# Optimization experiments

Measured on AMD Instinct MI355X. Metric: run time of the kernel, lower is better.

Reference implementation:

```python
import jax, jax.numpy as jnp
import numpy as np

BS, D, L, H = 8, 256, 1024, 8
DK = D // H
EPS = 1e-8


def setup_inputs() -> dict:
    key = jax.random.key(0)
    ks = jax.random.split(key, 9)
    queries = jax.random.normal(ks[0], (BS, D, L), jnp.float32)
    keys = jax.random.normal(ks[1], (BS, D, L), jnp.float32)
    values = jax.random.normal(ks[2], (BS, D, L), jnp.float32)
    # binary float mask over positions, (bs, L, 1) as the module expects
    mask = (jax.random.uniform(ks[3], (BS, L, 1)) > 0.1).astype(jnp.float32)
    # grouped 1x1 conv weights: one (dk, dk) block per head (xavier-ish scale)
    wscale = np.sqrt(2.0 / (DK + DK)).astype(np.float32)
    Wq = jax.random.normal(ks[4], (H, DK, DK), jnp.float32) * wscale
    Wk = jax.random.normal(ks[5], (H, DK, DK), jnp.float32) * wscale
    Wv = jax.random.normal(ks[6], (H, DK, DK), jnp.float32) * wscale
    # full 1x1 conv projection
    Wp = jax.random.normal(ks[7], (D, D), jnp.float32) * np.sqrt(1.0 / D).astype(np.float32)
    bp = jnp.zeros((D,), jnp.float32)
    return {"queries": queries, "keys": keys, "values": values, "mask": mask,
            "Wq": Wq, "Wk": Wk, "Wv": Wv, "Wp": Wp, "bp": bp}


def _grouped_conv1x1(x, W):
    # x: (bs, D, L) viewed as (bs, H, dk, L); W: (H, dk_out, dk_in)
    bs, _, l = x.shape
    xh = x.reshape(bs, H, DK, l)
    return jnp.einsum('hij,bhjl->bhil', W, xh)  # (bs, H, dk, L)


def _masked_softmax(logits, mask4):
    # logits: (bs, H, L, L); mask4: (bs, 1, 1, L) -- faithful to module's custom softmax
    max_value = jax.lax.stop_gradient(jnp.max(logits * mask4, axis=-1, keepdims=True))
    z = (logits - max_value) * mask4
    m = jnp.exp(z) * mask4
    n = jnp.sum(m, axis=-1, keepdims=True)
    p_mask = mask4 * jnp.swapaxes(mask4, 2, 3)  # (bs, 1, L, L)
    return p_mask * (m / (n + EPS))


def reference(queries, keys, values, mask, Wq, Wk, Wv, Wp, bp):
    bs, c, l = queries.shape
    m = jnp.swapaxes(mask, 1, 2)          # (bs, 1, L)
    m4 = m[:, :, None, :]                  # (bs, 1, 1, L)
    q = _grouped_conv1x1(queries, Wq) * m4  # (bs, H, dk, L)
    k = _grouped_conv1x1(keys, Wk) * m4
    v = _grouped_conv1x1(values, Wv)
    # attn[b,h,d,e] = sum_c q[b,h,c,d] k[b,h,c,e]  (no 1/sqrt(dk) scaling, as in source)
    attn = jnp.einsum('bhcd,bhce->bhde', q, k)
    atn = _masked_softmax(attn, m4)
    # value[b,h,c,k] = sum_d atn[b,h,k,d] * (v*mask)[b,h,c,d]
    val = jnp.einsum('bhkd,bhcd->bhck', atn, v * m4)
    val = val.reshape(bs, c, l)
    out = jnp.einsum('ij,bjl->bil', Wp, val) + bp[None, :, None]
    return jnp.swapaxes(out * m, 1, 2)      # (bs, L, D)
```

## Files before the change

kernel.cpp:

```cpp
#include <hip/hip_runtime.h>
#include <math.h>


constexpr int cD  = 256;
constexpr int cL  = 1024;
constexpr int cH  = 8;
constexpr int cDK = 32;

typedef __attribute__((ext_vector_type(8))) short s8v;
typedef __attribute__((ext_vector_type(4))) float f4v;
typedef unsigned int u32;
typedef unsigned short u16;

static __device__ __forceinline__ u32 rne_hi(float x) {
    u32 u = __float_as_uint(x);
    return u + 0x7fffu + ((u >> 16) & 1u);
}
static __device__ __forceinline__ u32 pack_bf2(float a, float b) {
    return __builtin_amdgcn_perm(rne_hi(b), rne_hi(a), 0x07060302u);
}
static __device__ __forceinline__ u16 f2bf(float x) { return (u16)(rne_hi(x) >> 16); }
static __device__ __forceinline__ float bf2f(u16 h) { return __uint_as_float(((u32)h) << 16); }

__global__ __launch_bounds__(256, 4) void proj_kv_kernel(
    const float* __restrict__ keys, const float* __restrict__ values,
    const float* __restrict__ mask, const float* __restrict__ Wk,
    const float* __restrict__ Wv, u16* __restrict__ kp_hi,
    u16* __restrict__ kp_lo, u16* __restrict__ vp_bf)
{
    __shared__ __align__(16) float xs[32][68];
    __shared__ __align__(16) float wT[32][36];
    __shared__ float msl[64];

    const int t   = threadIdx.x;
    const int bid = blockIdx.x;
    const int lt  = bid & 15;
    const int h   = (bid >> 4) & 7;
    const int b   = bid >> 7;
    const int l0  = lt * 64;

    if (t < 64) msl[t] = mask[b * cL + l0 + t];

    for (int idx = t; idx < 512; idx += 256) {
        int j = idx >> 4, l4 = (idx & 15) * 4;
        *reinterpret_cast<float4*>(&xs[j][l4]) =
            *reinterpret_cast<const float4*>(&keys[(b * cD + h * cDK + j) * cL + l0 + l4]);
    }
    for (int idx = t; idx < 1024; idx += 256) {
        int c = idx >> 5, j = idx & 31;
        wT[j][c] = Wk[(h * cDK + c) * cDK + j];
    }
    __syncthreads();
    {
        const int l = t & 63, ig = t >> 6;
        float acc[8] = {0, 0, 0, 0, 0, 0, 0, 0};
        #pragma unroll
        for (int j = 0; j < 32; ++j) {
            float xv = xs[j][l];
            float4 w0 = *reinterpret_cast<const float4*>(&wT[j][ig * 8]);
            float4 w1 = *reinterpret_cast<const float4*>(&wT[j][ig * 8 + 4]);
            acc[0] += w0.x * xv; acc[1] += w0.y * xv;
            acc[2] += w0.z * xv; acc[3] += w0.w * xv;
            acc[4] += w1.x * xv; acc[5] += w1.y * xv;
            acc[6] += w1.z * xv; acc[7] += w1.w * xv;
        }
        float mk = msl[l];
        s8v hv, lv;
        #pragma unroll
        for (int i = 0; i < 8; ++i) {
            float kv = acc[i] * mk;
            u16 hh = f2bf(kv);
            hv[i] = (short)hh;
            lv[i] = (short)f2bf(kv - bf2f(hh));
        }
        size_t off = (((size_t)(b * cH + h)) * cL + l0 + l) * cDK + ig * 8;
        *reinterpret_cast<s8v*>(&kp_hi[off]) = hv;
        *reinterpret_cast<s8v*>(&kp_lo[off]) = lv;
    }
    __syncthreads();

    for (int idx = t; idx < 512; idx += 256) {
        int j = idx >> 4, l4 = (idx & 15) * 4;
        *reinterpret_cast<float4*>(&xs[j][l4]) =
            *reinterpret_cast<const float4*>(&values[(b * cD + h * cDK + j) * cL + l0 + l4]);
    }
    for (int idx = t; idx < 1024; idx += 256) {
        int c = idx >> 5, j = idx & 31;
        wT[j][c] = Wv[(h * cDK + c) * cDK + j];
    }
    __syncthreads();
    {
        const int l4 = (t & 15) * 4;
        const int c0 = (t >> 4) * 2;
        float a0[4] = {0, 0, 0, 0}, a1[4] = {0, 0, 0, 0};
        #pragma unroll
        for (int j = 0; j < 32; ++j) {
            float4 xv = *reinterpret_cast<const float4*>(&xs[j][l4]);
            float w0 = wT[j][c0], w1 = wT[j][c0 + 1];
            a0[0] += w0 * xv.x; a0[1] += w0 * xv.y; a0[2] += w0 * xv.z; a0[3] += w0 * xv.w;
            a1[0] += w1 * xv.x; a1[1] += w1 * xv.y; a1[2] += w1 * xv.z; a1[3] += w1 * xv.w;
        }
        size_t base = ((size_t)(b * cH + h)) * cDK;
        uint2 v0 = make_uint2(pack_bf2(a0[0], a0[1]), pack_bf2(a0[2], a0[3]));
        uint2 v1 = make_uint2(pack_bf2(a1[0], a1[1]), pack_bf2(a1[2], a1[3]));
        *reinterpret_cast<uint2*>(&vp_bf[(base + c0) * cL + l0 + l4])     = v0;
        *reinterpret_cast<uint2*>(&vp_bf[(base + c0 + 1) * cL + l0 + l4]) = v1;
    }
}

__global__ __launch_bounds__(256, 3) void attn_kernel(
    const float* __restrict__ queries, const float* __restrict__ mask,
    const float* __restrict__ Wq, const u16* __restrict__ kp_hi,
    const u16* __restrict__ kp_lo, const u16* __restrict__ vp_bf,
    u16* __restrict__ val_bf)
{
    __shared__ __align__(16) u16 ksbuf[2][2][2048];
    __shared__ __align__(16) u16 qsb[2][2048];
    __shared__ __align__(16) u16 vsbuf[2][2304];
    __shared__ __align__(16) u32 pb32[2304];
    __shared__ __align__(16) float msbuf[2][64];

    const int t     = threadIdx.x;
    const int bid   = blockIdx.x;
    const int strip = bid & 15;
    const int h     = (bid >> 4) & 7;
    const int b     = bid >> 7;
    const int r0    = strip * 64;
    const int lane  = t & 63;
    const int w     = t >> 6;
    const int ln15  = lane & 15;
    const int lq    = lane >> 4;

    float* qtmp = reinterpret_cast<float*>(&ksbuf[0][0][0]);
    float* wqt  = reinterpret_cast<float*>((char*)&ksbuf[0][0][0] + 8704);
    {
        int j = t >> 3, f8 = (t & 7) * 8;
        const float* src = &queries[(b * cD + h * cDK + j) * cL + r0 + f8];
        float4 v0 = *reinterpret_cast<const float4*>(src);
        float4 v1 = *reinterpret_cast<const float4*>(src + 4);
        *reinterpret_cast<float4*>(&qtmp[j * 68 + f8])     = v0;
        *reinterpret_cast<float4*>(&qtmp[j * 68 + f8 + 4]) = v1;
    }
    {
        int c = t >> 3, j4 = (t & 7) * 4;
        float4 wv = *reinterpret_cast<const float4*>(&Wq[(h * cDK + c) * cDK + j4]);
        wqt[(j4 + 0) * 32 + c] = wv.x; wqt[(j4 + 1) * 32 + c] = wv.y;
        wqt[(j4 + 2) * 32 + c] = wv.z; wqt[(j4 + 3) * 32 + c] = wv.w;
    }
    __syncthreads();

    {
        float acc[8] = {0, 0, 0, 0, 0, 0, 0, 0};
        #pragma unroll
        for (int j = 0; j < 32; ++j) {
            float xv = qtmp[j * 68 + lane];
            float4 w0 = *reinterpret_cast<const float4*>(&wqt[j * 32 + w * 8]);
            float4 w1 = *reinterpret_cast<const float4*>(&wqt[j * 32 + w * 8 + 4]);
            acc[0] += w0.x * xv; acc[1] += w0.y * xv;
            acc[2] += w0.z * xv; acc[3] += w0.w * xv;
            acc[4] += w1.x * xv; acc[5] += w1.y * xv;
            acc[6] += w1.z * xv; acc[7] += w1.w * xv;
        }
        s8v hv, lv;
        #pragma unroll
        for (int i = 0; i < 8; ++i) {
            u16 hh = f2bf(acc[i]);
            hv[i] = (short)hh;
            lv[i] = (short)f2bf(acc[i] - bf2f(hh));
        }
        *reinterpret_cast<s8v*>(&qsb[0][lane * 32 + w * 8]) = hv;
        *reinterpret_cast<s8v*>(&qsb[1][lane * 32 + w * 8]) = lv;
    }
    __syncthreads();

    const size_t kvbase = ((size_t)(b * cH + h)) * 32768;
    const int se = t >> 2, sc = (t & 3) * 8;
    const int vc = t >> 3, ve = (t & 7) * 8;

    {
        s8v kh = *reinterpret_cast<const s8v*>(&kp_hi[kvbase + se * 32 + sc]);
        s8v kl = *reinterpret_cast<const s8v*>(&kp_lo[kvbase + se * 32 + sc]);
        *reinterpret_cast<s8v*>(&ksbuf[0][0][se * 32 + sc]) = kh;
        *reinterpret_cast<s8v*>(&ksbuf[0][1][se * 32 + sc]) = kl;
        s8v vv = *reinterpret_cast<const s8v*>(&vp_bf[kvbase + vc * 1024 + ve]);
        *reinterpret_cast<s8v*>(&vsbuf[0][vc * 72 + ve]) = vv;
        if (t < 64) msbuf[0][t] = mask[b * cL + t];
    }

    const s8v qh = *reinterpret_cast<const s8v*>(&qsb[0][(w * 16 + ln15) * 32 + lq * 8]);
    const s8v ql = *reinterpret_cast<const s8v*>(&qsb[1][(w * 16 + ln15) * 32 + lq * 8]);

    f4v o0 = {0.f, 0.f, 0.f, 0.f}, o1 = {0.f, 0.f, 0.f, 0.f};
    float mo = -INFINITY, lr = 0.f;
    const int pbrow = (w * 16 + ln15) * 36;
    const int ksoff = ln15 * 32 + lq * 8;
    const int vsoff = ln15 * 72 + lq * 8;

    for (int et = 0; et < 16; ++et) {
        __syncthreads();
        const int pp = et & 1;
        const bool pre = (et < 15);
        s8v khp, klp, vvp; float msp = 0.f;
        if (pre) {
            const int e0n = (et + 1) * 64;
            khp = *reinterpret_cast<const s8v*>(&kp_hi[kvbase + (e0n + se) * 32 + sc]);
            klp = *reinterpret_cast<const s8v*>(&kp_lo[kvbase + (e0n + se) * 32 + sc]);
            vvp = *reinterpret_cast<const s8v*>(&vp_bf[kvbase + vc * 1024 + e0n + ve]);
            if (t < 64) msp = mask[b * cL + e0n + t];
        }

        f4v sA[4];
        #pragma unroll
        for (int es = 0; es < 4; ++es) {
            const s8v kh = *reinterpret_cast<const s8v*>(&ksbuf[pp][0][es * 512 + ksoff]);
            const s8v kl = *reinterpret_cast<const s8v*>(&ksbuf[pp][1][es * 512 + ksoff]);
            f4v a = {0.f, 0.f, 0.f, 0.f};
            a = __builtin_amdgcn_mfma_f32_16x16x32_bf16(kh, qh, a, 0, 0, 0);
            a = __builtin_amdgcn_mfma_f32_16x16x32_bf16(kl, qh, a, 0, 0, 0);
            a = __builtin_amdgcn_mfma_f32_16x16x32_bf16(kh, ql, a, 0, 0, 0);
            sA[es] = a;
        }

        float tm = fmaxf(fmaxf(fmaxf(sA[0][0], sA[0][1]), fmaxf(sA[0][2], sA[0][3])),
                   fmaxf(fmaxf(fmaxf(sA[1][0], sA[1][1]), fmaxf(sA[1][2], sA[1][3])),
                   fmaxf(fmaxf(fmaxf(sA[2][0], sA[2][1]), fmaxf(sA[2][2], sA[2][3])),
                         fmaxf(fmaxf(sA[3][0], sA[3][1]), fmaxf(sA[3][2], sA[3][3])))));
        tm = fmaxf(tm, __shfl_xor(tm, 16));
        tm = fmaxf(tm, __shfl_xor(tm, 32));
        const float mn = fmaxf(mo, tm);
        const float al = __expf(mo - mn);
        mo = mn;
        o0[0] *= al; o0[1] *= al; o0[2] *= al; o0[3] *= al;
        o1[0] *= al; o1[1] *= al; o1[2] *= al; o1[3] *= al;

        float ps = 0.f;
        #pragma unroll
        for (int es = 0; es < 4; ++es) {
            float4 mk4 = *reinterpret_cast<const float4*>(&msbuf[pp][es * 16 + lq * 4]);
            float p0 = __expf((sA[es][0] - mn) * mk4.x) * mk4.x;
            float p1 = __expf((sA[es][1] - mn) * mk4.y) * mk4.y;
            float p2 = __expf((sA[es][2] - mn) * mk4.z) * mk4.z;
            float p3 = __expf((sA[es][3] - mn) * mk4.w) * mk4.w;
            ps += (p0 + p1) + (p2 + p3);
            uint2 pk = make_uint2(pack_bf2(p0, p1), pack_bf2(p2, p3));
            *reinterpret_cast<uint2*>(&pb32[pbrow + es * 8 + lq * 2]) = pk;
        }
        ps += __shfl_xor(ps, 16);
        ps += __shfl_xor(ps, 32);
        lr = lr * al + ps;

        #pragma unroll
        for (int ch = 0; ch < 2; ++ch) {
            s8v pB  = *reinterpret_cast<const s8v*>(
                          reinterpret_cast<const u16*>(&pb32[pbrow + ch * 16 + lq * 4]));
            s8v vA0 = *reinterpret_cast<const s8v*>(&vsbuf[pp][vsoff + ch * 32]);
            s8v vA1 = *reinterpret_cast<const s8v*>(&vsbuf[pp][vsoff + ch * 32 + 1152]);
            o0 = __builtin_amdgcn_mfma_f32_16x16x32_bf16(vA0, pB, o0, 0, 0, 0);
            o1 = __builtin_amdgcn_mfma_f32_16x16x32_bf16(vA1, pB, o1, 0, 0, 0);
        }

        if (pre) {
            const int bn = pp ^ 1;
            *reinterpret_cast<s8v*>(&ksbuf[bn][0][se * 32 + sc]) = khp;
            *reinterpret_cast<s8v*>(&ksbuf[bn][1][se * 32 + sc]) = klp;
            *reinterpret_cast<s8v*>(&vsbuf[bn][vc * 72 + ve]) = vvp;
            if (t < 64) msbuf[bn][t] = msp;
        }
    }

    {
        const float linv = 1.0f / (lr + 1e-8f);
        const size_t obase = ((size_t)(b * cL + r0 + w * 16 + ln15)) * cD + h * cDK;
        uint2 q0 = make_uint2(pack_bf2(o0[0] * linv, o0[1] * linv),
                              pack_bf2(o0[2] * linv, o0[3] * linv));
        uint2 q1 = make_uint2(pack_bf2(o1[0] * linv, o1[1] * linv),
                              pack_bf2(o1[2] * linv, o1[3] * linv));
        *reinterpret_cast<uint2*>(&val_bf[obase + lq * 4])      = q0;
        *reinterpret_cast<uint2*>(&val_bf[obase + 16 + lq * 4]) = q1;
    }
}

__global__ __launch_bounds__(256, 2) void outproj_kernel(
    const u16* __restrict__ val_bf, const float* __restrict__ Wp,
    const float* __restrict__ bp, const float* __restrict__ mask,
    float* __restrict__ out)
{
    __shared__ __align__(16) u16 vt[64 * 264];
    __shared__ __align__(16) u16 wpb[64 * 264];
    __shared__ float mrow[64];

    const int t    = threadIdx.x;
    const int bid  = blockIdx.x;
    const int it   = bid & 3;
    const int lt   = (bid >> 2) & 15;
    const int b    = bid >> 6;
    const int l0   = lt * 64, i0 = it * 64;
    const int lane = t & 63, w = t >> 6, ln15 = lane & 15, lq = lane >> 4;

    {
        int row = t >> 2, seg = (t & 3) * 64;
        const u16* src = &val_bf[((size_t)(b * cL + l0 + row)) * cD + seg];
        #pragma unroll
        for (int k = 0; k < 4; ++k) {
            s8v a0 = *reinterpret_cast<const s8v*>(src + k * 16);
            s8v a1 = *reinterpret_cast<const s8v*>(src + k * 16 + 8);
            *reinterpret_cast<s8v*>(&vt[row * 264 + seg + k * 16])     = a0;
            *reinterpret_cast<s8v*>(&vt[row * 264 + seg + k * 16 + 8]) = a1;
        }
    }
    {
        int row = t >> 2, seg = (t & 3) * 64;
        const float* src = &Wp[((size_t)(i0 + row)) * cD + seg];
        #pragma unroll
        for (int k = 0; k < 8; ++k) {
            float4 f0 = *reinterpret_cast<const float4*>(src + k * 8);
            float4 f1 = *reinterpret_cast<const float4*>(src + k * 8 + 4);
            uint4 pk = make_uint4(pack_bf2(f0.x, f0.y), pack_bf2(f0.z, f0.w),
                                  pack_bf2(f1.x, f1.y), pack_bf2(f1.z, f1.w));
            *reinterpret_cast<uint4*>(&wpb[row * 264 + seg + k * 8]) = pk;
        }
    }
    if (t < 64) mrow[t] = mask[b * cL + l0 + t];
    __syncthreads();

    f4v acc[4] = {{0.f, 0.f, 0.f, 0.f}, {0.f, 0.f, 0.f, 0.f},
                  {0.f, 0.f, 0.f, 0.f}, {0.f, 0.f, 0.f, 0.f}};
    #pragma unroll
    for (int kc = 0; kc < 8; ++kc) {
        s8v aA = *reinterpret_cast<const s8v*>(&vt[(w * 16 + ln15) * 264 + kc * 32 + lq * 8]);
        #pragma unroll
        for (int ti = 0; ti < 4; ++ti) {
            s8v bB = *reinterpret_cast<const s8v*>(&wpb[(ti * 16 + ln15) * 264 + kc * 32 + lq * 8]);
            acc[ti] = __builtin_amdgcn_mfma_f32_16x16x32_bf16(aA, bB, acc[ti], 0, 0, 0);
        }
    }

    float mk[4];
    #pragma unroll
    for (int rg = 0; rg < 4; ++rg) mk[rg] = mrow[w * 16 + lq * 4 + rg];
    #pragma unroll
    for (int ti = 0; ti < 4; ++ti) {
        float bpv = bp[i0 + ti * 16 + ln15];
        #pragma unroll
        for (int rg = 0; rg < 4; ++rg) {
            int l = l0 + w * 16 + lq * 4 + rg;
            out[((size_t)(b * cL + l)) * cD + i0 + ti * 16 + ln15] =
                (acc[ti][rg] + bpv) * mk[rg];
        }
    }
}

extern "C" void kernel_launch(void* const* d_in, const int* in_sizes, int n_in,
                              void* d_out, int out_size, void* d_ws, size_t ws_size,
                              hipStream_t stream) {
    const float* queries = (const float*)d_in[0];
    const float* keys    = (const float*)d_in[1];
    const float* values  = (const float*)d_in[2];
    const float* mask    = (const float*)d_in[3];
    const float* Wq      = (const float*)d_in[4];
    const float* Wk      = (const float*)d_in[5];
    const float* Wv      = (const float*)d_in[6];
    const float* Wp      = (const float*)d_in[7];
    const float* bp      = (const float*)d_in[8];
    float* out = (float*)d_out;

    char* wsb = (char*)d_ws;
    u16* kp_hi  = (u16*)(wsb);
    u16* kp_lo  = (u16*)(wsb + (4u << 20));
    u16* vp_bf  = (u16*)(wsb + (8u << 20));
    u16* val_bf = (u16*)(wsb + (12u << 20));

    proj_kv_kernel<<<dim3(1024), dim3(256), 0, stream>>>(keys, values, mask, Wk, Wv,
                                                         kp_hi, kp_lo, vp_bf);
    attn_kernel<<<dim3(1024), dim3(256), 0, stream>>>(queries, mask, Wq,
                                                      kp_hi, kp_lo, vp_bf, val_bf);
    outproj_kernel<<<dim3(512), dim3(256), 0, stream>>>(val_bf, Wp, bp, mask, out);
}
```

Baseline: 145.0 us.

## Switch attention pipeline from split bf16 hi/lo to single fp16 MFMA

Replaces the bf16 hi+lo split representation of Q and K (three MFMAs per score tile) with a single fp16 representation and one f16 MFMA per tile. This drops the kp_lo buffer and its loads and stores, and converts V, P, val and Wp to fp16. It also restructures the shared-memory layout into one padded arena, preloads the full mask row once, and raises the attention kernel's occupancy hint from 3 to 4. fp16 has less exponent range than bf16, and the unscaled logits now carry less precision than the compensated split did, so accuracy may degrade.

```diff
diff --git a/kernel.cpp b/kernel.cpp
--- a/kernel.cpp
+++ b/kernel.cpp
@@ -7,26 +7,16 @@
 constexpr int cH  = 8;
 constexpr int cDK = 32;
 
-typedef __attribute__((ext_vector_type(8))) short s8v;
+typedef _Float16 f16;
+typedef __attribute__((ext_vector_type(8))) _Float16 h8;
+typedef __attribute__((ext_vector_type(4))) _Float16 h4;
 typedef __attribute__((ext_vector_type(4))) float f4v;
-typedef unsigned int u32;
-typedef unsigned short u16;
-
-static __device__ __forceinline__ u32 rne_hi(float x) {
-    u32 u = __float_as_uint(x);
-    return u + 0x7fffu + ((u >> 16) & 1u);
-}
-static __device__ __forceinline__ u32 pack_bf2(float a, float b) {
-    return __builtin_amdgcn_perm(rne_hi(b), rne_hi(a), 0x07060302u);
-}
-static __device__ __forceinline__ u16 f2bf(float x) { return (u16)(rne_hi(x) >> 16); }
-static __device__ __forceinline__ float bf2f(u16 h) { return __uint_as_float(((u32)h) << 16); }
 
 __global__ __launch_bounds__(256, 4) void proj_kv_kernel(
     const float* __restrict__ keys, const float* __restrict__ values,
     const float* __restrict__ mask, const float* __restrict__ Wk,
-    const float* __restrict__ Wv, u16* __restrict__ kp_hi,
-    u16* __restrict__ kp_lo, u16* __restrict__ vp_bf)
+    const float* __restrict__ Wv, f16* __restrict__ kp_h,
+    f16* __restrict__ vp_h)
 {
     __shared__ __align__(16) float xs[32][68];
     __shared__ __align__(16) float wT[32][36];
@@ -52,7 +42,7 @@
     }
     __syncthreads();
     {
-        const int l = t & 63, ig = t >> 6;
+        const int l = t >> 2, ig = t & 3;
         float acc[8] = {0, 0, 0, 0, 0, 0, 0, 0};
         #pragma unroll
         for (int j = 0; j < 32; ++j) {
@@ -65,17 +55,11 @@
             acc[6] += w1.z * xv; acc[7] += w1.w * xv;
         }
         float mk = msl[l];
-        s8v hv, lv;
-        #pragma unroll
-        for (int i = 0; i < 8; ++i) {
-            float kv = acc[i] * mk;
-            u16 hh = f2bf(kv);
-            hv[i] = (short)hh;
-            lv[i] = (short)f2bf(kv - bf2f(hh));
-        }
+        h8 hv;
+        #pragma unroll
+        for (int i = 0; i < 8; ++i) hv[i] = (f16)(acc[i] * mk);
         size_t off = (((size_t)(b * cH + h)) * cL + l0 + l) * cDK + ig * 8;
-        *reinterpret_cast<s8v*>(&kp_hi[off]) = hv;
-        *reinterpret_cast<s8v*>(&kp_lo[off]) = lv;
+        *reinterpret_cast<h8*>(&kp_h[off]) = hv;
     }
     __syncthreads();
 
@@ -101,24 +85,27 @@
             a1[0] += w1 * xv.x; a1[1] += w1 * xv.y; a1[2] += w1 * xv.z; a1[3] += w1 * xv.w;
         }
         size_t base = ((size_t)(b * cH + h)) * cDK;
-        uint2 v0 = make_uint2(pack_bf2(a0[0], a0[1]), pack_bf2(a0[2], a0[3]));
-        uint2 v1 = make_uint2(pack_bf2(a1[0], a1[1]), pack_bf2(a1[2], a1[3]));
-        *reinterpret_cast<uint2*>(&vp_bf[(base + c0) * cL + l0 + l4])     = v0;
-        *reinterpret_cast<uint2*>(&vp_bf[(base + c0 + 1) * cL + l0 + l4]) = v1;
+        h4 v0, v1;
+        #pragma unroll
+        for (int i = 0; i < 4; ++i) { v0[i] = (f16)a0[i]; v1[i] = (f16)a1[i]; }
+        *reinterpret_cast<h4*>(&vp_h[(base + c0) * cL + l0 + l4])     = v0;
+        *reinterpret_cast<h4*>(&vp_h[(base + c0 + 1) * cL + l0 + l4]) = v1;
     }
 }
 
-__global__ __launch_bounds__(256, 3) void attn_kernel(
+__global__ __launch_bounds__(256, 4) void attn_kernel(
     const float* __restrict__ queries, const float* __restrict__ mask,
-    const float* __restrict__ Wq, const u16* __restrict__ kp_hi,
-    const u16* __restrict__ kp_lo, const u16* __restrict__ vp_bf,
-    u16* __restrict__ val_bf)
+    const float* __restrict__ Wq, const f16* __restrict__ kp_h,
+    const f16* __restrict__ vp_h, f16* __restrict__ val_h)
 {
-    __shared__ __align__(16) u16 ksbuf[2][2][2048];
-    __shared__ __align__(16) u16 qsb[2][2048];
-    __shared__ __align__(16) u16 vsbuf[2][2304];
-    __shared__ __align__(16) u32 pb32[2304];
-    __shared__ __align__(16) float msbuf[2][64];
+    __shared__ __align__(16) char smem[37888];
+    f16*   ks    = (f16*)smem;
+    f16*   vsb   = (f16*)(smem + 10240);
+    f16*   qsb   = (f16*)(smem + 19456);
+    f16*   pbf   = (f16*)(smem + 24576);
+    float* msall = (float*)(smem + 33792);
+    float* qtmp  = (float*)smem;
+    float* wqt   = (float*)(smem + 8704);
 
     const int t     = threadIdx.x;
     const int bid   = blockIdx.x;
@@ -131,8 +118,6 @@
     const int ln15  = lane & 15;
     const int lq    = lane >> 4;
 
-    float* qtmp = reinterpret_cast<float*>(&ksbuf[0][0][0]);
-    float* wqt  = reinterpret_cast<float*>((char*)&ksbuf[0][0][0] + 8704);
     {
         int j = t >> 3, f8 = (t & 7) * 8;
         const float* src = &queries[(b * cD + h * cDK + j) * cL + r0 + f8];
@@ -147,6 +132,8 @@
         wqt[(j4 + 0) * 32 + c] = wv.x; wqt[(j4 + 1) * 32 + c] = wv.y;
         wqt[(j4 + 2) * 32 + c] = wv.z; wqt[(j4 + 3) * 32 + c] = wv.w;
     }
+    *reinterpret_cast<float4*>(&msall[t * 4]) =
+        *reinterpret_cast<const float4*>(&mask[b * cL + t * 4]);
     __syncthreads();
 
     {
@@ -161,64 +148,49 @@
             acc[4] += w1.x * xv; acc[5] += w1.y * xv;
             acc[6] += w1.z * xv; acc[7] += w1.w * xv;
         }
-        s8v hv, lv;
-        #pragma unroll
-        for (int i = 0; i < 8; ++i) {
-            u16 hh = f2bf(acc[i]);
-            hv[i] = (short)hh;
-            lv[i] = (short)f2bf(acc[i] - bf2f(hh));
-        }
-        *reinterpret_cast<s8v*>(&qsb[0][lane * 32 + w * 8]) = hv;
-        *reinterpret_cast<s8v*>(&qsb[1][lane * 32 + w * 8]) = lv;
+        h8 hv;
+        #pragma unroll
+        for (int i = 0; i < 8; ++i) hv[i] = (f16)acc[i];
+        *reinterpret_cast<h8*>(&qsb[lane * 40 + w * 8]) = hv;
     }
     __syncthreads();
 
     const size_t kvbase = ((size_t)(b * cH + h)) * 32768;
-    const int se = t >> 2, sc = (t & 3) * 8;
-    const int vc = t >> 3, ve = (t & 7) * 8;
-
-    {
-        s8v kh = *reinterpret_cast<const s8v*>(&kp_hi[kvbase + se * 32 + sc]);
-        s8v kl = *reinterpret_cast<const s8v*>(&kp_lo[kvbase + se * 32 + sc]);
-        *reinterpret_cast<s8v*>(&ksbuf[0][0][se * 32 + sc]) = kh;
-        *reinterpret_cast<s8v*>(&ksbuf[0][1][se * 32 + sc]) = kl;
-        s8v vv = *reinterpret_cast<const s8v*>(&vp_bf[kvbase + vc * 1024 + ve]);
-        *reinterpret_cast<s8v*>(&vsbuf[0][vc * 72 + ve]) = vv;
-        if (t < 64) msbuf[0][t] = mask[b * cL + t];
-    }
-
-    const s8v qh = *reinterpret_cast<const s8v*>(&qsb[0][(w * 16 + ln15) * 32 + lq * 8]);
-    const s8v ql = *reinterpret_cast<const s8v*>(&qsb[1][(w * 16 + ln15) * 32 + lq * 8]);
+    const int se = t >> 2, sb = (t & 3) * 8;
+    const int vc = t >> 3, veb = (t & 7) * 8;
+
+    {
+        h8 kh = *reinterpret_cast<const h8*>(&kp_h[kvbase + se * 32 + sb]);
+        *reinterpret_cast<h8*>(&ks[se * 40 + sb]) = kh;
+        h8 vv = *reinterpret_cast<const h8*>(&vp_h[kvbase + vc * 1024 + veb]);
+        *reinterpret_cast<h8*>(&vsb[vc * 72 + veb]) = vv;
+    }
+
+    const h8 qf = *reinterpret_cast<const h8*>(&qsb[(w * 16 + ln15) * 40 + lq * 8]);
 
     f4v o0 = {0.f, 0.f, 0.f, 0.f}, o1 = {0.f, 0.f, 0.f, 0.f};
     float mo = -INFINITY, lr = 0.f;
-    const int pbrow = (w * 16 + ln15) * 36;
-    const int ksoff = ln15 * 32 + lq * 8;
+    const int prow  = (w * 16 + ln15) * 72;
     const int vsoff = ln15 * 72 + lq * 8;
 
     for (int et = 0; et < 16; ++et) {
         __syncthreads();
         const int pp = et & 1;
         const bool pre = (et < 15);
-        s8v khp, klp, vvp; float msp = 0.f;
+        h8 khp, vvp;
         if (pre) {
             const int e0n = (et + 1) * 64;
-            khp = *reinterpret_cast<const s8v*>(&kp_hi[kvbase + (e0n + se) * 32 + sc]);
-            klp = *reinterpret_cast<const s8v*>(&kp_lo[kvbase + (e0n + se) * 32 + sc]);
-            vvp = *reinterpret_cast<const s8v*>(&vp_bf[kvbase + vc * 1024 + e0n + ve]);
-            if (t < 64) msp = mask[b * cL + e0n + t];
+            khp = *reinterpret_cast<const h8*>(&kp_h[kvbase + (e0n + se) * 32 + sb]);
+            vvp = *reinterpret_cast<const h8*>(&vp_h[kvbase + vc * 1024 + e0n + veb]);
         }
 
         f4v sA[4];
         #pragma unroll
         for (int es = 0; es < 4; ++es) {
-            const s8v kh = *reinterpret_cast<const s8v*>(&ksbuf[pp][0][es * 512 + ksoff]);
-            const s8v kl = *reinterpret_cast<const s8v*>(&ksbuf[pp][1][es * 512 + ksoff]);
-            f4v a = {0.f, 0.f, 0.f, 0.f};
-            a = __builtin_amdgcn_mfma_f32_16x16x32_bf16(kh, qh, a, 0, 0, 0);
-            a = __builtin_amdgcn_mfma_f32_16x16x32_bf16(kl, qh, a, 0, 0, 0);
-            a = __builtin_amdgcn_mfma_f32_16x16x32_bf16(kh, ql, a, 0, 0, 0);
-            sA[es] = a;
+            const h8 kf = *reinterpret_cast<const h8*>(
+                &ks[pp * 2560 + (es * 16 + ln15) * 40 + lq * 8]);
+            f4v z = {0.f, 0.f, 0.f, 0.f};
+            sA[es] = __builtin_amdgcn_mfma_f32_16x16x32_f16(kf, qf, z, 0, 0, 0);
         }
 
         float tm = fmaxf(fmaxf(fmaxf(sA[0][0], sA[0][1]), fmaxf(sA[0][2], sA[0][3])),
@@ -236,14 +208,14 @@
         float ps = 0.f;
         #pragma unroll
         for (int es = 0; es < 4; ++es) {
-            float4 mk4 = *reinterpret_cast<const float4*>(&msbuf[pp][es * 16 + lq * 4]);
+            float4 mk4 = *reinterpret_cast<const float4*>(&msall[et * 64 + es * 16 + lq * 4]);
             float p0 = __expf((sA[es][0] - mn) * mk4.x) * mk4.x;
             float p1 = __expf((sA[es][1] - mn) * mk4.y) * mk4.y;
             float p2 = __expf((sA[es][2] - mn) * mk4.z) * mk4.z;
             float p3 = __expf((sA[es][3] - mn) * mk4.w) * mk4.w;
             ps += (p0 + p1) + (p2 + p3);
-            uint2 pk = make_uint2(pack_bf2(p0, p1), pack_bf2(p2, p3));
-            *reinterpret_cast<uint2*>(&pb32[pbrow + es * 8 + lq * 2]) = pk;
+            h4 pk; pk[0] = (f16)p0; pk[1] = (f16)p1; pk[2] = (f16)p2; pk[3] = (f16)p3;
+            *reinterpret_cast<h4*>(&pbf[prow + es * 16 + lq * 4]) = pk;
         }
         ps += __shfl_xor(ps, 16);
         ps += __shfl_xor(ps, 32);
@@ -251,42 +223,40 @@
 
         #pragma unroll
         for (int ch = 0; ch < 2; ++ch) {
-            s8v pB  = *reinterpret_cast<const s8v*>(
-                          reinterpret_cast<const u16*>(&pb32[pbrow + ch * 16 + lq * 4]));
-            s8v vA0 = *reinterpret_cast<const s8v*>(&vsbuf[pp][vsoff + ch * 32]);
-            s8v vA1 = *reinterpret_cast<const s8v*>(&vsbuf[pp][vsoff + ch * 32 + 1152]);
-            o0 = __builtin_amdgcn_mfma_f32_16x16x32_bf16(vA0, pB, o0, 0, 0, 0);
-            o1 = __builtin_amdgcn_mfma_f32_16x16x32_bf16(vA1, pB, o1, 0, 0, 0);
+            h8 pf  = *reinterpret_cast<const h8*>(&pbf[prow + ch * 32 + lq * 8]);
+            h8 va0 = *reinterpret_cast<const h8*>(&vsb[pp * 2304 + vsoff + ch * 32]);
+            h8 va1 = *reinterpret_cast<const h8*>(&vsb[pp * 2304 + vsoff + ch * 32 + 1152]);
+            o0 = __builtin_amdgcn_mfma_f32_16x16x32_f16(va0, pf, o0, 0, 0, 0);
+            o1 = __builtin_amdgcn_mfma_f32_16x16x32_f16(va1, pf, o1, 0, 0, 0);
         }
 
         if (pre) {
-            const int bn = pp ^ 1;
-            *reinterpret_cast<s8v*>(&ksbuf[bn][0][se * 32 + sc]) = khp;
-            *reinterpret_cast<s8v*>(&ksbuf[bn][1][se * 32 + sc]) = klp;
-            *reinterpret_cast<s8v*>(&vsbuf[bn][vc * 72 + ve]) = vvp;
-            if (t < 64) msbuf[bn][t] = msp;
+            *reinterpret_cast<h8*>(&ks[(pp ^ 1) * 2560 + se * 40 + sb]) = khp;
+            *reinterpret_cast<h8*>(&vsb[(pp ^ 1) * 2304 + vc * 72 + veb]) = vvp;
         }
     }
 
     {
         const float linv = 1.0f / (lr + 1e-8f);
         const size_t obase = ((size_t)(b * cL + r0 + w * 16 + ln15)) * cD + h * cDK;
-        uint2 q0 = make_uint2(pack_bf2(o0[0] * linv, o0[1] * linv),
-                              pack_bf2(o0[2] * linv, o0[3] * linv));
-        uint2 q1 = make_uint2(pack_bf2(o1[0] * linv, o1[1] * linv),
-                              pack_bf2(o1[2] * linv, o1[3] * linv));
-        *reinterpret_cast<uint2*>(&val_bf[obase + lq * 4])      = q0;
-        *reinterpret_cast<uint2*>(&val_bf[obase + 16 + lq * 4]) = q1;
+        h4 q0, q1;
+        #pragma unroll
+        for (int i = 0; i < 4; ++i) {
+            q0[i] = (f16)(o0[i] * linv);
+            q1[i] = (f16)(o1[i] * linv);
+        }
+        *reinterpret_cast<h4*>(&val_h[obase + lq * 4])      = q0;
+        *reinterpret_cast<h4*>(&val_h[obase + 16 + lq * 4]) = q1;
     }
 }
 
 __global__ __launch_bounds__(256, 2) void outproj_kernel(
-    const u16* __restrict__ val_bf, const float* __restrict__ Wp,
+    const f16* __restrict__ val_h, const float* __restrict__ Wp,
     const float* __restrict__ bp, const float* __restrict__ mask,
     float* __restrict__ out)
 {
-    __shared__ __align__(16) u16 vt[64 * 264];
-    __shared__ __align__(16) u16 wpb[64 * 264];
+    __shared__ __align__(16) f16 vt[64 * 264];
+    __shared__ __align__(16) f16 wpb[64 * 264];
     __shared__ float mrow[64];
 
     const int t    = threadIdx.x;
@@ -298,26 +268,24 @@
     const int lane = t & 63, w = t >> 6, ln15 = lane & 15, lq = lane >> 4;
 
     {
-        int row = t >> 2, seg = (t & 3) * 64;
-        const u16* src = &val_bf[((size_t)(b * cL + l0 + row)) * cD + seg];
-        #pragma unroll
-        for (int k = 0; k < 4; ++k) {
-            s8v a0 = *reinterpret_cast<const s8v*>(src + k * 16);
-            s8v a1 = *reinterpret_cast<const s8v*>(src + k * 16 + 8);
-            *reinterpret_cast<s8v*>(&vt[row * 264 + seg + k * 16])     = a0;
-            *reinterpret_cast<s8v*>(&vt[row * 264 + seg + k * 16 + 8]) = a1;
-        }
-    }
-    {
-        int row = t >> 2, seg = (t & 3) * 64;
+        int row = t & 63, seg = (t >> 6) * 64;
+        const f16* src = &val_h[((size_t)(b * cL + l0 + row)) * cD + seg];
+        #pragma unroll
+        for (int k = 0; k < 8; ++k)
+            *reinterpret_cast<h8*>(&vt[row * 264 + seg + k * 8]) =
+                *reinterpret_cast<const h8*>(src + k * 8);
+    }
+    {
+        int row = t & 63, seg = (t >> 6) * 64;
         const float* src = &Wp[((size_t)(i0 + row)) * cD + seg];
         #pragma unroll
         for (int k = 0; k < 8; ++k) {
             float4 f0 = *reinterpret_cast<const float4*>(src + k * 8);
             float4 f1 = *reinterpret_cast<const float4*>(src + k * 8 + 4);
-            uint4 pk = make_uint4(pack_bf2(f0.x, f0.y), pack_bf2(f0.z, f0.w),
-                                  pack_bf2(f1.x, f1.y), pack_bf2(f1.z, f1.w));
-            *reinterpret_cast<uint4*>(&wpb[row * 264 + seg + k * 8]) = pk;
+            h8 hv;
+            hv[0] = (f16)f0.x; hv[1] = (f16)f0.y; hv[2] = (f16)f0.z; hv[3] = (f16)f0.w;
+            hv[4] = (f16)f1.x; hv[5] = (f16)f1.y; hv[6] = (f16)f1.z; hv[7] = (f16)f1.w;
+            *reinterpret_cast<h8*>(&wpb[row * 264 + seg + k * 8]) = hv;
         }
     }
     if (t < 64) mrow[t] = mask[b * cL + l0 + t];
@@ -327,11 +295,11 @@
                   {0.f, 0.f, 0.f, 0.f}, {0.f, 0.f, 0.f, 0.f}};
     #pragma unroll
     for (int kc = 0; kc < 8; ++kc) {
-        s8v aA = *reinterpret_cast<const s8v*>(&vt[(w * 16 + ln15) * 264 + kc * 32 + lq * 8]);
+        h8 aA = *reinterpret_cast<const h8*>(&vt[(w * 16 + ln15) * 264 + kc * 32 + lq * 8]);
         #pragma unroll
         for (int ti = 0; ti < 4; ++ti) {
-            s8v bB = *reinterpret_cast<const s8v*>(&wpb[(ti * 16 + ln15) * 264 + kc * 32 + lq * 8]);
-            acc[ti] = __builtin_amdgcn_mfma_f32_16x16x32_bf16(aA, bB, acc[ti], 0, 0, 0);
+            h8 bB = *reinterpret_cast<const h8*>(&wpb[(ti * 16 + ln15) * 264 + kc * 32 + lq * 8]);
+            acc[ti] = __builtin_amdgcn_mfma_f32_16x16x32_f16(aA, bB, acc[ti], 0, 0, 0);
         }
     }
 
@@ -365,14 +333,13 @@
     float* out = (float*)d_out;
 
     char* wsb = (char*)d_ws;
-    u16* kp_hi  = (u16*)(wsb);
-    u16* kp_lo  = (u16*)(wsb + (4u << 20));
-    u16* vp_bf  = (u16*)(wsb + (8u << 20));
-    u16* val_bf = (u16*)(wsb + (12u << 20));
+    f16* kp_h  = (f16*)(wsb);
+    f16* vp_h  = (f16*)(wsb + (4u << 20));
+    f16* val_h = (f16*)(wsb + (8u << 20));
 
     proj_kv_kernel<<<dim3(1024), dim3(256), 0, stream>>>(keys, values, mask, Wk, Wv,
-                                                         kp_hi, kp_lo, vp_bf);
+                                                         kp_h, vp_h);
     attn_kernel<<<dim3(1024), dim3(256), 0, stream>>>(queries, mask, Wq,
-                                                      kp_hi, kp_lo, vp_bf, val_bf);
-    outproj_kernel<<<dim3(512), dim3(256), 0, stream>>>(val_bf, Wp, bp, mask, out);
+                                                      kp_h, vp_h, val_h);
+    outproj_kernel<<<dim3(512), dim3(256), 0, stream>>>(val_h, Wp, bp, mask, out);
 }
```

Result: faster. 131.7 us (-9.2%).
